# Kernel optimization log

Measured on AMD Instinct MI355X. Metric: run time of the kernel, lower is better.

## Reference

```python
import jax, jax.numpy as jnp
import numpy as np
from functools import partial

INPUT_DIM = 22
HIDDEN = 64
LAYERS = 3
OUT = 4
B, T = 1024, 512


def _lstm_layer(x_seq, w_ih, w_hh, b_ih, b_hh):
    # x_seq: [B, T, Din]; gate order (PyTorch): i, f, g, o
    Bsz = x_seq.shape[0]
    H = w_hh.shape[1]
    # precompute input projections for all timesteps: [B, T, 4H]
    x_proj = jnp.einsum('bti,gi->btg', x_seq, w_ih) + b_ih + b_hh

    def step(carry, xp):
        h, c = carry
        gates = xp + h @ w_hh.T  # [B, 4H]
        i, f, g, o = jnp.split(gates, 4, axis=-1)
        i = jax.nn.sigmoid(i)
        f = jax.nn.sigmoid(f)
        g = jnp.tanh(g)
        o = jax.nn.sigmoid(o)
        c = f * c + i * g
        h = o * jnp.tanh(c)
        return (h, c), h

    init = (jnp.zeros((Bsz, H), x_seq.dtype), jnp.zeros((Bsz, H), x_seq.dtype))
    _, hs = jax.lax.scan(step, init, jnp.swapaxes(x_proj, 0, 1))  # [T, B, H]
    return jnp.swapaxes(hs, 0, 1)  # [B, T, H]


def setup_inputs() -> dict:
    key = jax.random.key(0)
    ks = jax.random.split(key, 16)
    inp = {'x': jax.random.normal(ks[0], (B, INPUT_DIM, T), dtype=jnp.float32)}
    k = 1.0 / np.sqrt(HIDDEN)
    i = 1
    for l in range(LAYERS):
        din = INPUT_DIM if l == 0 else HIDDEN
        inp[f'w_ih{l}'] = jax.random.uniform(ks[i], (4 * HIDDEN, din), minval=-k, maxval=k); i += 1
        inp[f'w_hh{l}'] = jax.random.uniform(ks[i], (4 * HIDDEN, HIDDEN), minval=-k, maxval=k); i += 1
        inp[f'b_ih{l}'] = jax.random.uniform(ks[i], (4 * HIDDEN,), minval=-k, maxval=k); i += 1
        inp[f'b_hh{l}'] = jax.random.uniform(ks[i], (4 * HIDDEN,), minval=-k, maxval=k); i += 1
    inp['w_fc'] = jax.random.uniform(ks[i], (OUT, HIDDEN), minval=-k, maxval=k); i += 1
    inp['b_fc'] = jax.random.uniform(ks[i], (OUT,), minval=-k, maxval=k)
    return inp


def reference(x, w_ih0, w_hh0, b_ih0, b_hh0, w_ih1, w_hh1, b_ih1, b_hh1,
              w_ih2, w_hh2, b_ih2, b_hh2, w_fc, b_fc):
    # x: [B, 22, T] -> batch_first [B, T, 22]
    h = jnp.transpose(x, (0, 2, 1))
    h = _lstm_layer(h, w_ih0, w_hh0, b_ih0, b_hh0)
    # inter-layer dropout(0.4) is identity in eval/inference mode
    h = _lstm_layer(h, w_ih1, w_hh1, b_ih1, b_hh1)
    h = _lstm_layer(h, w_ih2, w_hh2, b_ih2, b_hh2)
    last = h[:, -1, :]  # [B, H]
    return last @ w_fc.T + b_fc  # [B, 4]
```

## Files before the change

kernel.cpp:

```cpp
#include <hip/hip_runtime.h>


#define TT   512
#define NTH  768
#define NBLK 256

typedef _Float16 h16;
typedef __attribute__((ext_vector_type(8))) _Float16 h16x8;
typedef __attribute__((ext_vector_type(4))) float f32x4;

#define MFMA16(a, b, c) __builtin_amdgcn_mfma_f32_16x16x32_f16((a), (b), (c), 0, 0, 0)

__device__ __forceinline__ float sigm(float z) {
    return __builtin_amdgcn_rcpf(1.f + __expf(-z));
}

__device__ __forceinline__ h16x8 loadB(const float* __restrict__ W, int ld, int ro,
                                       int k0, int kmax) {
    h16x8 r;
    #pragma unroll
    for (int i = 0; i < 8; ++i) {
        const int k = k0 + i;
        r[i] = (h16)((k < kmax) ? W[(size_t)ro * ld + k] : 0.f);
    }
    return r;
}

struct TrueC  { static constexpr bool value = true;  };
struct FalseC { static constexpr bool value = false; };

__global__ __attribute__((amdgpu_flat_work_group_size(NTH, NTH), amdgpu_waves_per_eu(3)))
void lstm_mfma(
    const float* __restrict__ x,
    const float* __restrict__ wih0, const float* __restrict__ whh0,
    const float* __restrict__ bih0, const float* __restrict__ bhh0,
    const float* __restrict__ wih1, const float* __restrict__ whh1,
    const float* __restrict__ bih1, const float* __restrict__ bhh1,
    const float* __restrict__ wih2, const float* __restrict__ whh2,
    const float* __restrict__ bih2, const float* __restrict__ bhh2,
    const float* __restrict__ wfc, const float* __restrict__ bfc,
    float* __restrict__ out)
{
    const int tid  = threadIdx.x;
    const int w    = tid >> 6;
    const int wl   = w >> 2;
    const int wg   = w & 3;
    const int lane = tid & 63;
    const int nloc = lane & 15;
    const int kg   = lane >> 4;
    const int b4   = blockIdx.x * 4;
    const int u    = wg * 16 + nloc;

    __shared__ alignas(16) h16 XL[2 * 32 * 512];
    __shared__ alignas(16) h16 HT[3 * 2 * 1024];
    __shared__ h16 PAD[3072];

    h16x8 Bf[4][4];
    float bias[4];
    #pragma unroll
    for (int g = 0; g < 4; ++g) {
        const int ro = g * 64 + u;
        if (wl == 0) {
            Bf[g][0] = loadB(wih0, 22, ro, kg * 8,      22);
            Bf[g][1] = loadB(whh0, 64, ro, kg * 8,      64);
            Bf[g][2] = loadB(whh0, 64, ro, 32 + kg * 8, 64);
            Bf[g][3] = Bf[g][2];
            bias[g]  = bih0[ro] + bhh0[ro];
        } else if (wl == 1) {
            Bf[g][0] = loadB(wih1, 64, ro, kg * 8,      64);
            Bf[g][1] = loadB(wih1, 64, ro, 32 + kg * 8, 64);
            Bf[g][2] = loadB(whh1, 64, ro, kg * 8,      64);
            Bf[g][3] = loadB(whh1, 64, ro, 32 + kg * 8, 64);
            bias[g]  = bih1[ro] + bhh1[ro];
        } else {
            Bf[g][0] = loadB(wih2, 64, ro, kg * 8,      64);
            Bf[g][1] = loadB(wih2, 64, ro, 32 + kg * 8, 64);
            Bf[g][2] = loadB(whh2, 64, ro, kg * 8,      64);
            Bf[g][3] = loadB(whh2, 64, ro, 32 + kg * 8, 64);
            bias[g]  = bih2[ro] + bhh2[ro];
        }
    }

    if (bias[0] > 1.0e30f) { PAD[tid & 2047] = (h16)bias[0]; out[0] = (float)PAD[0]; }

    {
        int* xz = (int*)XL;
        for (int i = tid; i < 2 * 32 * 256; i += NTH) xz[i] = 0;
        int* hz = (int*)HT;
        for (int i = tid; i < 3 * 2 * 512; i += NTH) hz[i] = 0;
    }
    __syncthreads();

    auto stage_x = [&](int chunk) {
        if (tid < 4 * 22) {
            const int bl = tid / 22, ii = tid - bl * 22;
            const float* src = x + (size_t)(b4 + bl) * (22 * 512) + (size_t)ii * 512
                                 + chunk * 32;
            h16* dst = &XL[(chunk & 1) * (32 * 512) + (ii >> 3) * 128 + (4 * bl) * 8 + (ii & 7)];
            #pragma unroll
            for (int q = 0; q < 8; ++q) {
                const float4 v = ((const float4*)src)[q];
                dst[(q * 4 + 0) * 512] = (h16)v.x;
                dst[(q * 4 + 1) * 512] = (h16)v.y;
                dst[(q * 4 + 2) * 512] = (h16)v.z;
                dst[(q * 4 + 3) * 512] = (h16)v.w;
            }
        }
    };
    stage_x(0);

    const int lo8  = lane * 8;
    const int hoff = (u >> 3) * 128 + kg * 32 + (u & 7);

    float cst = 0.f;

    auto ew = [&](const f32x4& zi, const f32x4& zf, const f32x4& zg, const f32x4& zo,
                  h16* hb) {
        const float vi = sigm(zi[0]);
        const float vf = sigm(zf[0]);
        const float vg = 2.f * sigm(2.f * zg[0]) - 1.f;
        const float vo = sigm(zo[0]);
        const float c  = vf * cst + vi * vg;
        cst = c;
        hb[hoff] = (h16)(vo * (2.f * sigm(2.f * c) - 1.f));
    };

    f32x4 zb[4];
    #pragma unroll
    for (int g = 0; g < 4; ++g) zb[g] = f32x4{bias[g], 0.f, 0.f, 0.f};

    __syncthreads();

    f32x4 zc[4];
    if (wl == 0) {
        const h16x8 ax0 = *(const h16x8*)&XL[lo8];
        #pragma unroll
        for (int g = 0; g < 4; ++g) zc[g] = MFMA16(ax0, Bf[g][0], zb[g]);
    } else {
        #pragma unroll
        for (int g = 0; g < 4; ++g) zc[g] = zb[g];
    }

    auto tick = [&](int t, auto edgec) {
        constexpr bool EDGE = decltype(edgec)::value;
        const int wb = t & 1, rb = wb ^ 1;
        const h16* h0r = HT + 0 * 2048 + rb * 1024;
        h16*       h0w = HT + 0 * 2048 + wb * 1024;
        const h16* h1r = HT + 1 * 2048 + rb * 1024;
        h16*       h1w = HT + 1 * 2048 + wb * 1024;
        const h16* h2r = HT + 2 * 2048 + rb * 1024;
        h16*       h2w = HT + 2 * 2048 + wb * 1024;

        if (wl == 0) {
            const bool sa = !EDGE || (t < TT);
            const bool ia = !EDGE || (t < TT - 1);
            f32x4 z[4];
            h16x8 a0lo, a0hi, axn;
            if (sa) {
                a0lo = *(const h16x8*)(h0r + lo8);
                a0hi = *(const h16x8*)(h0r + lo8 + 512);
            }
            if (ia) {
                const int tn = t + 1;
                axn = *(const h16x8*)&XL[((tn >> 5) & 1) * (32 * 512) + (tn & 31) * 512 + lo8];
            }
            if (sa) {
                #pragma unroll
                for (int g = 0; g < 4; ++g) {
                    z[g] = MFMA16(a0lo, Bf[g][1], zc[g]);
                    z[g] = MFMA16(a0hi, Bf[g][2], z[g]);
                }
            }
            if ((t & 31) == 16 && (t >> 5) < 15) stage_x((t >> 5) + 1);
            if (sa) ew(z[0], z[1], z[2], z[3], h0w);
            if (ia) {
                #pragma unroll
                for (int g = 0; g < 4; ++g)
                    zc[g] = MFMA16(axn, Bf[g][0], zb[g]);
            }
        } else if (wl == 1) {
            const bool sa = !EDGE || (t >= 2 && t < TT + 2);
            const bool ia = !EDGE || (t >= 1 && t < TT + 1);
            f32x4 z[4];
            h16x8 a1lo, a1hi, a0lo, a0hi;
            if (sa) {
                a1lo = *(const h16x8*)(h1r + lo8);
                a1hi = *(const h16x8*)(h1r + lo8 + 512);
            }
            if (ia) {
                a0lo = *(const h16x8*)(h0r + lo8);
                a0hi = *(const h16x8*)(h0r + lo8 + 512);
            }
            if (sa) {
                #pragma unroll
                for (int g = 0; g < 4; ++g) {
                    z[g] = MFMA16(a1lo, Bf[g][2], zc[g]);
                    z[g] = MFMA16(a1hi, Bf[g][3], z[g]);
                }
            }
            if (sa) ew(z[0], z[1], z[2], z[3], h1w);
            if (ia) {
                #pragma unroll
                for (int g = 0; g < 4; ++g) {
                    f32x4 zn = MFMA16(a0lo, Bf[g][0], zb[g]);
                    zc[g] = MFMA16(a0hi, Bf[g][1], zn);
                }
            }
        } else {
            const bool sa = !EDGE || (t >= 4);
            const bool ia = !EDGE || (t >= 3 && t < TT + 3);
            f32x4 z[4];
            h16x8 a2lo, a2hi, a1lo, a1hi;
            if (sa) {
                a2lo = *(const h16x8*)(h2r + lo8);
                a2hi = *(const h16x8*)(h2r + lo8 + 512);
            }
            if (ia) {
                a1lo = *(const h16x8*)(h1r + lo8);
                a1hi = *(const h16x8*)(h1r + lo8 + 512);
            }
            if (sa) {
                #pragma unroll
                for (int g = 0; g < 4; ++g) {
                    z[g] = MFMA16(a2lo, Bf[g][2], zc[g]);
                    z[g] = MFMA16(a2hi, Bf[g][3], z[g]);
                }
            }
            if (sa) ew(z[0], z[1], z[2], z[3], h2w);
            if (ia) {
                #pragma unroll
                for (int g = 0; g < 4; ++g) {
                    f32x4 zn = MFMA16(a1lo, Bf[g][0], zb[g]);
                    zc[g] = MFMA16(a1hi, Bf[g][1], zn);
                }
            }
        }
        __syncthreads();
    };

    #pragma unroll 1
    for (int t = 0; t < 4; ++t) tick(t, TrueC{});
    #pragma unroll 1
    for (int t = 4; t < TT - 1; ++t) tick(t, FalseC{});
    #pragma unroll 1
    for (int t = TT - 1; t < TT + 4; ++t) tick(t, TrueC{});

    if (tid < 16) {
        const int ms = tid >> 2, o = tid & 3;
        const h16* h2 = HT + 2 * 2048 + 1024;
        float acc = bfc[o];
        #pragma unroll 1
        for (int uu = 0; uu < 64; ++uu)
            acc += (float)h2[(uu >> 3) * 128 + (4 * ms) * 8 + (uu & 7)] * wfc[o * 64 + uu];
        out[(b4 + ms) * 4 + o] = acc;
    }
}

extern "C" void kernel_launch(void* const* d_in, const int* in_sizes, int n_in,
                              void* d_out, int out_size, void* d_ws, size_t ws_size,
                              hipStream_t stream) {
    const float* x    = (const float*)d_in[0];
    const float* wih0 = (const float*)d_in[1];
    const float* whh0 = (const float*)d_in[2];
    const float* bih0 = (const float*)d_in[3];
    const float* bhh0 = (const float*)d_in[4];
    const float* wih1 = (const float*)d_in[5];
    const float* whh1 = (const float*)d_in[6];
    const float* bih1 = (const float*)d_in[7];
    const float* bhh1 = (const float*)d_in[8];
    const float* wih2 = (const float*)d_in[9];
    const float* whh2 = (const float*)d_in[10];
    const float* bih2 = (const float*)d_in[11];
    const float* bhh2 = (const float*)d_in[12];
    const float* wfc  = (const float*)d_in[13];
    const float* bfc  = (const float*)d_in[14];
    float* out = (float*)d_out;

    lstm_mfma<<<dim3(NBLK), dim3(NTH), 0, stream>>>(
        x, wih0, whh0, bih0, bhh0, wih1, whh1, bih1, bhh1,
        wih2, whh2, bih2, bhh2, wfc, bfc, out);
}
```

Baseline: 395.8 us.

## Compact LDS layout for hidden and input tiles, loading only active MFMA rows

Replaces the zero-padded 16-row MFMA A-operand LDS layout for hidden states and staged input with a compact 4-row layout using padded strides. Only the lanes that carry real batch rows (lane&3==0) now issue LDS reads; the other lanes keep zero fragments held in registers. This cuts LDS footprint and read traffic on the per-timestep critical path and simplifies the final FC readback. The PAD array is enlarged, apparently to keep total LDS usage, and therefore occupancy, unchanged. The change adds divergent conditional loads and relies on the zero-initialized fragments staying zero.

```diff
diff --git a/kernel.cpp b/kernel.cpp
--- a/kernel.cpp
+++ b/kernel.cpp
@@ -4,6 +4,13 @@
 #define TT   512
 #define NTH  768
 #define NBLK 256
+
+#define XSTR  40
+#define XSLAB (4 * XSTR)
+#define XCH   (32 * XSLAB)
+#define HSTR  72
+#define HBUF  (4 * HSTR)
+#define HLAY  (2 * HBUF)
 
 typedef _Float16 h16;
 typedef __attribute__((ext_vector_type(8))) _Float16 h16x8;
@@ -51,9 +58,9 @@
     const int b4   = blockIdx.x * 4;
     const int u    = wg * 16 + nloc;
 
-    __shared__ alignas(16) h16 XL[2 * 32 * 512];
-    __shared__ alignas(16) h16 HT[3 * 2 * 1024];
-    __shared__ h16 PAD[3072];
+    __shared__ alignas(16) h16 XL[2 * XCH];
+    __shared__ alignas(16) h16 HT[3 * HLAY];
+    __shared__ h16 PAD[30720];
 
     h16x8 Bf[4][4];
     float bias[4];
@@ -85,9 +92,9 @@
 
     {
         int* xz = (int*)XL;
-        for (int i = tid; i < 2 * 32 * 256; i += NTH) xz[i] = 0;
+        for (int i = tid; i < XCH; i += NTH) xz[i] = 0;
         int* hz = (int*)HT;
-        for (int i = tid; i < 3 * 2 * 512; i += NTH) hz[i] = 0;
+        for (int i = tid; i < (3 * HLAY) / 2; i += NTH) hz[i] = 0;
     }
     __syncthreads();
 
@@ -96,21 +103,23 @@
             const int bl = tid / 22, ii = tid - bl * 22;
             const float* src = x + (size_t)(b4 + bl) * (22 * 512) + (size_t)ii * 512
                                  + chunk * 32;
-            h16* dst = &XL[(chunk & 1) * (32 * 512) + (ii >> 3) * 128 + (4 * bl) * 8 + (ii & 7)];
+            h16* dst = &XL[(chunk & 1) * XCH + bl * XSTR + ii];
             #pragma unroll
             for (int q = 0; q < 8; ++q) {
                 const float4 v = ((const float4*)src)[q];
-                dst[(q * 4 + 0) * 512] = (h16)v.x;
-                dst[(q * 4 + 1) * 512] = (h16)v.y;
-                dst[(q * 4 + 2) * 512] = (h16)v.z;
-                dst[(q * 4 + 3) * 512] = (h16)v.w;
+                dst[(q * 4 + 0) * XSLAB] = (h16)v.x;
+                dst[(q * 4 + 1) * XSLAB] = (h16)v.y;
+                dst[(q * 4 + 2) * XSLAB] = (h16)v.z;
+                dst[(q * 4 + 3) * XSLAB] = (h16)v.w;
             }
         }
     };
     stage_x(0);
 
-    const int lo8  = lane * 8;
-    const int hoff = (u >> 3) * 128 + kg * 32 + (u & 7);
+    const int j     = lane >> 2;
+    const int hro   = (j & 3) * HSTR + (j >> 2) * 8;
+    const int xro   = (j & 3) * XSTR + (j >> 2) * 8;
+    const int hoffp = kg * HSTR + u;
 
     float cst = 0.f;
 
@@ -122,20 +131,24 @@
         const float vo = sigm(zo[0]);
         const float c  = vf * cst + vi * vg;
         cst = c;
-        hb[hoff] = (h16)(vo * (2.f * sigm(2.f * c) - 1.f));
+        hb[hoffp] = (h16)(vo * (2.f * sigm(2.f * c) - 1.f));
     };
 
     f32x4 zb[4];
     #pragma unroll
     for (int g = 0; g < 4; ++g) zb[g] = f32x4{bias[g], 0.f, 0.f, 0.f};
 
+    h16x8 fx = {};
+    h16x8 fslo = {}, fshi = {};
+    h16x8 fulo = {}, fuhi = {};
+
     __syncthreads();
 
     f32x4 zc[4];
     if (wl == 0) {
-        const h16x8 ax0 = *(const h16x8*)&XL[lo8];
+        if ((lane & 3) == 0) fx = *(const h16x8*)&XL[xro];
         #pragma unroll
-        for (int g = 0; g < 4; ++g) zc[g] = MFMA16(ax0, Bf[g][0], zb[g]);
+        for (int g = 0; g < 4; ++g) zc[g] = MFMA16(fx, Bf[g][0], zb[g]);
     } else {
         #pragma unroll
         for (int g = 0; g < 4; ++g) zc[g] = zb[g];
@@ -144,31 +157,32 @@
     auto tick = [&](int t, auto edgec) {
         constexpr bool EDGE = decltype(edgec)::value;
         const int wb = t & 1, rb = wb ^ 1;
-        const h16* h0r = HT + 0 * 2048 + rb * 1024;
-        h16*       h0w = HT + 0 * 2048 + wb * 1024;
-        const h16* h1r = HT + 1 * 2048 + rb * 1024;
-        h16*       h1w = HT + 1 * 2048 + wb * 1024;
-        const h16* h2r = HT + 2 * 2048 + rb * 1024;
-        h16*       h2w = HT + 2 * 2048 + wb * 1024;
+        const h16* h0r = HT + 0 * HLAY + rb * HBUF;
+        h16*       h0w = HT + 0 * HLAY + wb * HBUF;
+        const h16* h1r = HT + 1 * HLAY + rb * HBUF;
+        h16*       h1w = HT + 1 * HLAY + wb * HBUF;
+        const h16* h2r = HT + 2 * HLAY + rb * HBUF;
+        h16*       h2w = HT + 2 * HLAY + wb * HBUF;
 
         if (wl == 0) {
             const bool sa = !EDGE || (t < TT);
             const bool ia = !EDGE || (t < TT - 1);
             f32x4 z[4];
-            h16x8 a0lo, a0hi, axn;
+            if ((lane & 3) == 0) {
+                if (sa) {
+                    fslo = *(const h16x8*)(h0r + hro);
+                    fshi = *(const h16x8*)(h0r + hro + 32);
+                }
+                if (ia) {
+                    const int tn = t + 1;
+                    fx = *(const h16x8*)&XL[((tn >> 5) & 1) * XCH + (tn & 31) * XSLAB + xro];
+                }
+            }
             if (sa) {
-                a0lo = *(const h16x8*)(h0r + lo8);
-                a0hi = *(const h16x8*)(h0r + lo8 + 512);
-            }
-            if (ia) {
-                const int tn = t + 1;
-                axn = *(const h16x8*)&XL[((tn >> 5) & 1) * (32 * 512) + (tn & 31) * 512 + lo8];
-            }
-            if (sa) {
-                #pragma unroll
-                for (int g = 0; g < 4; ++g) {
-                    z[g] = MFMA16(a0lo, Bf[g][1], zc[g]);
-                    z[g] = MFMA16(a0hi, Bf[g][2], z[g]);
+                #pragma unroll
+                for (int g = 0; g < 4; ++g) {
+                    z[g] = MFMA16(fslo, Bf[g][1], zc[g]);
+                    z[g] = MFMA16(fshi, Bf[g][2], z[g]);
                 }
             }
             if ((t & 31) == 16 && (t >> 5) < 15) stage_x((t >> 5) + 1);
@@ -176,65 +190,68 @@
             if (ia) {
                 #pragma unroll
                 for (int g = 0; g < 4; ++g)
-                    zc[g] = MFMA16(axn, Bf[g][0], zb[g]);
+                    zc[g] = MFMA16(fx, Bf[g][0], zb[g]);
             }
         } else if (wl == 1) {
             const bool sa = !EDGE || (t >= 2 && t < TT + 2);
             const bool ia = !EDGE || (t >= 1 && t < TT + 1);
             f32x4 z[4];
-            h16x8 a1lo, a1hi, a0lo, a0hi;
+            if ((lane & 3) == 0) {
+                if (sa) {
+                    fslo = *(const h16x8*)(h1r + hro);
+                    fshi = *(const h16x8*)(h1r + hro + 32);
+                }
+                if (ia) {
+                    fulo = *(const h16x8*)(h0r + hro);
+                    fuhi = *(const h16x8*)(h0r + hro + 32);
+                }
+            }
             if (sa) {
-                a1lo = *(const h16x8*)(h1r + lo8);
-                a1hi = *(const h16x8*)(h1r + lo8 + 512);
-            }
-            if (ia) {
-                a0lo = *(const h16x8*)(h0r + lo8);
-                a0hi = *(const h16x8*)(h0r + lo8 + 512);
-            }
-            if (sa) {
-                #pragma unroll
-                for (int g = 0; g < 4; ++g) {
-                    z[g] = MFMA16(a1lo, Bf[g][2], zc[g]);
-                    z[g] = MFMA16(a1hi, Bf[g][3], z[g]);
+                #pragma unroll
+                for (int g = 0; g < 4; ++g) {
+                    z[g] = MFMA16(fslo, Bf[g][2], zc[g]);
+                    z[g] = MFMA16(fshi, Bf[g][3], z[g]);
                 }
             }
             if (sa) ew(z[0], z[1], z[2], z[3], h1w);
             if (ia) {
                 #pragma unroll
                 for (int g = 0; g < 4; ++g) {
-                    f32x4 zn = MFMA16(a0lo, Bf[g][0], zb[g]);
-                    zc[g] = MFMA16(a0hi, Bf[g][1], zn);
+                    f32x4 zn = MFMA16(fulo, Bf[g][0], zb[g]);
+                    zc[g] = MFMA16(fuhi, Bf[g][1], zn);
                 }
             }
         } else {
             const bool sa = !EDGE || (t >= 4);
             const bool ia = !EDGE || (t >= 3 && t < TT + 3);
             f32x4 z[4];
-            h16x8 a2lo, a2hi, a1lo, a1hi;
+            if ((lane & 3) == 0) {
+                if (sa) {
+                    fslo = *(const h16x8*)(h2r + hro);
+                    fshi = *(const h16x8*)(h2r + hro + 32);
+                }
+                if (ia) {
+                    fulo = *(const h16x8*)(h1r + hro);
+                    fuhi = *(const h16x8*)(h1r + hro + 32);
+                }
+            }
             if (sa) {
-                a2lo = *(const h16x8*)(h2r + lo8);
-                a2hi = *(const h16x8*)(h2r + lo8 + 512);
-            }
-            if (ia) {
-                a1lo = *(const h16x8*)(h1r + lo8);
-                a1hi = *(const h16x8*)(h1r + lo8 + 512);
-            }
-            if (sa) {
-                #pragma unroll
-                for (int g = 0; g < 4; ++g) {
-                    z[g] = MFMA16(a2lo, Bf[g][2], zc[g]);
-                    z[g] = MFMA16(a2hi, Bf[g][3], z[g]);
+                #pragma unroll
+                for (int g = 0; g < 4; ++g) {
+                    z[g] = MFMA16(fslo, Bf[g][2], zc[g]);
+                    z[g] = MFMA16(fshi, Bf[g][3], z[g]);
                 }
             }
             if (sa) ew(z[0], z[1], z[2], z[3], h2w);
             if (ia) {
                 #pragma unroll
                 for (int g = 0; g < 4; ++g) {
-                    f32x4 zn = MFMA16(a1lo, Bf[g][0], zb[g]);
-                    zc[g] = MFMA16(a1hi, Bf[g][1], zn);
+                    f32x4 zn = MFMA16(fulo, Bf[g][0], zb[g]);
+                    zc[g] = MFMA16(fuhi, Bf[g][1], zn);
                 }
             }
         }
+
         __syncthreads();
     };
 
@@ -247,11 +264,11 @@
 
     if (tid < 16) {
         const int ms = tid >> 2, o = tid & 3;
-        const h16* h2 = HT + 2 * 2048 + 1024;
+        const h16* h2 = HT + 2 * HLAY + 1 * HBUF;
         float acc = bfc[o];
         #pragma unroll 1
         for (int uu = 0; uu < 64; ++uu)
-            acc += (float)h2[(uu >> 3) * 128 + (4 * ms) * 8 + (uu & 7)] * wfc[o * 64 + uu];
+            acc += (float)h2[ms * HSTR + uu] * wfc[o * 64 + uu];
         out[(b4 + ms) * 4 + o] = acc;
     }
 }
```

New measurement: 418.6 us. +5.8%, slower.
